# Kernel tuning notes

Hardware: AMD Instinct MI355X
Metric: run time of the kernel (lower is better)

The kernel has to match this reference:

```python
import jax, jax.numpy as jnp
import numpy as np

# DCNv2 config (matches init_kwargs)
STRIDE, PAD, DIL = 1, 1, 1
KH, KW = 3, 3
K = KH * KW


def setup_inputs() -> dict:
    key = jax.random.key(0)
    k1, k2, k3, k4 = jax.random.split(key, 4)
    B, C, H, W = 2, 256, 96, 96
    O = 256
    inp = jax.random.normal(k1, (B, C, H, W), jnp.float32)
    # offset channels interleaved (dy, dx) per kernel tap -> 2*K channels
    offset = jax.random.normal(k2, (B, 2 * K, H, W), jnp.float32)
    # modulation mask in [0,1) (sigmoid is applied outside this module in DCN heads)
    mask = jax.random.uniform(k3, (B, K, H, W), jnp.float32)
    n = C * KH * KW
    stdv = 1.0 / float(np.sqrt(n))
    weight = jax.random.uniform(k4, (O, C, KH, KW), jnp.float32, -stdv, stdv)
    bias = jnp.zeros((O,), jnp.float32)
    return {"input": inp, "offset": offset, "mask": mask, "weight": weight, "bias": bias}


def reference(input, offset, mask, weight, bias):
    B, C, H, W = input.shape
    O = weight.shape[0]
    Ho = (H + 2 * PAD - DIL * (KH - 1) - 1) // STRIDE + 1
    Wo = (W + 2 * PAD - DIL * (KW - 1) - 1) // STRIDE + 1

    # learned per-pixel offsets: channel layout [dy_k0, dx_k0, dy_k1, dx_k1, ...]
    dy = offset[:, 0::2]  # [B,K,Ho,Wo]
    dx = offset[:, 1::2]  # [B,K,Ho,Wo]

    ky = (jnp.arange(K) // KW * DIL).astype(jnp.float32)  # kernel tap row offsets
    kx = (jnp.arange(K) % KW * DIL).astype(jnp.float32)   # kernel tap col offsets
    base_y = (jnp.arange(Ho) * STRIDE - PAD).astype(jnp.float32)
    base_x = (jnp.arange(Wo) * STRIDE - PAD).astype(jnp.float32)

    # sampling positions, [B,K,Ho,Wo]
    y = base_y[None, None, :, None] + ky[None, :, None, None] + dy
    x = base_x[None, None, None, :] + kx[None, :, None, None] + dx

    y0 = jnp.floor(y)
    x0 = jnp.floor(x)
    wy = y - y0  # bilinear fractional weights
    wx = x - x0

    inp_flat = input.reshape(B, C, H * W)

    def gather(yi, xi):
        # zero-padded bilinear corner gather: out-of-bounds -> 0
        ii = yi.astype(jnp.int32)
        jj = xi.astype(jnp.int32)
        valid = ((ii >= 0) & (ii < H) & (jj >= 0) & (jj < W)).astype(input.dtype)
        idx = jnp.clip(ii, 0, H - 1) * W + jnp.clip(jj, 0, W - 1)  # [B,K,Ho,Wo]
        v = jnp.take_along_axis(inp_flat, idx.reshape(B, 1, -1), axis=2)  # [B,C,K*Ho*Wo]
        return v * valid.reshape(B, 1, -1)

    v00 = gather(y0, x0)
    v01 = gather(y0, x0 + 1)
    v10 = gather(y0 + 1, x0)
    v11 = gather(y0 + 1, x0 + 1)

    wyf = wy.reshape(B, 1, -1)
    wxf = wx.reshape(B, 1, -1)
    sampled = (v00 * (1 - wyf) * (1 - wxf) + v01 * (1 - wyf) * wxf
               + v10 * wyf * (1 - wxf) + v11 * wyf * wxf)  # [B,C,K*Ho*Wo]

    mod = sampled * mask.reshape(B, 1, -1)           # modulation per tap/pixel
    mod = mod.reshape(B, C, K, Ho * Wo)
    out = jnp.einsum('bcks,ock->bos', mod, weight.reshape(O, C, K)) + bias[None, :, None]
    return out.reshape(B, O, Ho, Wo)
```

## Files before the change

### kernel.cpp

```cpp
#include <hip/hip_runtime.h>
#include <hip/hip_bf16.h>


#define Hh 96
#define Ww 96
#define Cc 256
#define Oo 256
#define Bb 2
#define Kk 9
#define Ss (Hh * Ww)
#define CKTOT (Cc * Kk)

typedef __bf16 bf16x8 __attribute__((ext_vector_type(8)));
typedef __bf16 bf16x2v __attribute__((ext_vector_type(2)));
typedef float f32x16 __attribute__((ext_vector_type(16)));
typedef float f32x2 __attribute__((ext_vector_type(2)));

__device__ __forceinline__ f32x2 up2(unsigned u) {
  f32x2 r;
  r.x = __uint_as_float(u << 16);
  r.y = __uint_as_float(u & 0xffff0000u);
  return r;
}

__device__ __forceinline__ void barrier_lgkm() {
  asm volatile("" ::: "memory");
  __builtin_amdgcn_s_waitcnt(0xC07F);
  __builtin_amdgcn_s_barrier();
  asm volatile("" ::: "memory");
}

__global__ __launch_bounds__(256) void prep(const float* __restrict__ inp,
                                            const float* __restrict__ wsrc,
                                            __bf16* __restrict__ it,
                                            __bf16* __restrict__ wt) {
  __shared__ float tile[64][65];
  const int bx = blockIdx.x;
  const int tid = threadIdx.x;

  if (bx < 1152) {
    const int hw0 = (bx % 144) * 64;
    const int c0 = ((bx / 144) & 3) * 64;
    const int b = bx / 576;
    const int hw_l = tid & 63, cr = tid >> 6;
    const float* src = inp + ((size_t)(b * Cc + c0) * Ss) + hw0;
#pragma unroll
    for (int r = 0; r < 16; ++r) {
      int c_l = r * 4 + cr;
      tile[c_l][hw_l] = src[(size_t)c_l * Ss + hw_l];
    }
    __syncthreads();
    const int cp = (tid & 31) * 2, hr = tid >> 5;
    __bf16* dst = it + ((size_t)(b * Ss + hw0) * Cc) + c0;
#pragma unroll
    for (int r = 0; r < 8; ++r) {
      int hw_s = r * 8 + hr;
      bf16x2v p;
      p.x = (__bf16)tile[cp][hw_s];
      p.y = (__bf16)tile[cp + 1][hw_s];
      *(bf16x2v*)(dst + (size_t)hw_s * Cc + cp) = p;
    }
  } else {
    int i = (bx - 1152) * 256 + tid;
    int j = i & 7;
    int l = (i >> 3) & 63;
    int osub = (i >> 9) & 7;
    int cc = (i >> 12) & 15;
    int kk = i >> 16;
    int o = osub * 32 + (l & 31);
    int ch = cc * 16 + ((l >> 5) << 3) + j;
    wt[i] = (__bf16)wsrc[(o * Cc + ch) * Kk + kk];
  }
}

__global__ __launch_bounds__(256, 3) void dcn_main(
    const __bf16* __restrict__ it,
    const __bf16* __restrict__ wt,
    const float* __restrict__ offset,
    const float* __restrict__ mask,
    const float* __restrict__ bias,
    float* __restrict__ out)
{
  __shared__ __bf16 colT[2][32 * 256];
  __shared__ int4 pa9[9][32];
  __shared__ float4 pw9[9][32];

  const int tid = threadIdx.x;
  const int tile = (blockIdx.x & 7) * 36 + (blockIdx.x >> 3);
  const int s0 = tile * 32;
  const int b = blockIdx.y;
  const int lane = tid & 63;
  const int wv = tid >> 6;
  const int sB = lane & 31;
  const int hi = lane >> 5;
  const int fs = tid >> 3;
  const int fg = tid & 7;

  const __bf16* itb = it + (size_t)b * Ss * Cc;

  for (int idx = tid; idx < 9 * 32; idx += 256) {
    int kk = idx >> 5;
    int sl = idx & 31;
    int s = s0 + sl;
    int ho = s / Ww;
    int wo = s - ho * Ww;
    float dy = offset[((size_t)(b * 18 + 2 * kk)) * Ss + s];
    float dx = offset[((size_t)(b * 18 + 2 * kk + 1)) * Ss + s];
    float m = mask[((size_t)(b * 9 + kk)) * Ss + s];
    float y = (float)(ho - 1 + kk / 3) + dy;
    float x = (float)(wo - 1 + kk % 3) + dx;
    float fy = floorf(y), fx = floorf(x);
    int y0 = (int)fy, x0 = (int)fx;
    float wy = y - fy, wx = x - fx;
    int y1 = y0 + 1, x1 = x0 + 1;
    float vy0 = (y0 >= 0 && y0 < Hh) ? 1.f : 0.f;
    float vy1 = (y1 >= 0 && y1 < Hh) ? 1.f : 0.f;
    float vx0 = (x0 >= 0 && x0 < Ww) ? 1.f : 0.f;
    float vx1 = (x1 >= 0 && x1 < Ww) ? 1.f : 0.f;
    int y0c = min(max(y0, 0), Hh - 1), y1c = min(max(y1, 0), Hh - 1);
    int x0c = min(max(x0, 0), Ww - 1), x1c = min(max(x1, 0), Ww - 1);
    pa9[kk][sl] = make_int4((y0c * Ww + x0c) * Cc, (y0c * Ww + x1c) * Cc,
                            (y1c * Ww + x0c) * Cc, (y1c * Ww + x1c) * Cc);
    pw9[kk][sl] = make_float4(m * (1.f - wy) * (1.f - wx) * vy0 * vx0,
                              m * (1.f - wy) * wx * vy0 * vx1,
                              m * wy * (1.f - wx) * vy1 * vx0,
                              m * wy * wx * vy1 * vx1);
  }
  __syncthreads();

  f32x16 acc0, acc1;
#pragma unroll
  for (int j = 0; j < 16; ++j) { acc0[j] = 0.f; acc1[j] = 0.f; }

  auto ldW = [&](int kk, int cc, int which) {
    size_t idx = (size_t)((kk * 16 + cc) * 8 + wv * 2 + which);
    return *(const bf16x8*)(wt + (idx << 9) + (lane << 3));
  };
  auto ldB = [&](int buf, int cc) {
    int g = ((2 * cc + hi) ^ (sB & 7)) << 3;
    return *(const bf16x8*)(&colT[buf][sB * 256 + g]);
  };

  for (int kk = 0; kk < Kk; ++kk) {
    const int buf = kk & 1;
    {
      int4 a = pa9[kk][fs];
      float4 wq = pw9[kk][fs];
      __bf16* drow = &colT[buf][fs * 256];
#pragma unroll
      for (int it2 = 0; it2 < 4; ++it2) {
        int g = fg + it2 * 8;
        const __bf16* p = itb + g * 8;
        uint4 c00 = *(const uint4*)(p + a.x);
        uint4 c01 = *(const uint4*)(p + a.y);
        uint4 c10 = *(const uint4*)(p + a.z);
        uint4 c11 = *(const uint4*)(p + a.w);
        unsigned u0[4] = {c00.x, c00.y, c00.z, c00.w};
        unsigned u1[4] = {c01.x, c01.y, c01.z, c01.w};
        unsigned u2[4] = {c10.x, c10.y, c10.z, c10.w};
        unsigned u3[4] = {c11.x, c11.y, c11.z, c11.w};
        bf16x8 rv;
#pragma unroll
        for (int w = 0; w < 4; ++w) {
          f32x2 r = up2(u0[w]) * wq.x + up2(u1[w]) * wq.y +
                    up2(u2[w]) * wq.z + up2(u3[w]) * wq.w;
          rv[2 * w] = (__bf16)r.x;
          rv[2 * w + 1] = (__bf16)r.y;
        }
        *(bf16x8*)(drow + ((g ^ (fs & 7)) << 3)) = rv;
      }
    }
    bf16x8 Wacur = ldW(kk, 0, 0);
    bf16x8 Wbcur = ldW(kk, 0, 1);
    barrier_lgkm();

    bf16x8 Bcur = ldB(buf, 0);
#pragma unroll
    for (int cc = 0; cc < 16; ++cc) {
      bf16x8 Bn, Wan, Wbn;
      if (cc < 15) {
        Bn = ldB(buf, cc + 1);
        Wan = ldW(kk, cc + 1, 0);
        Wbn = ldW(kk, cc + 1, 1);
      }
      acc0 = __builtin_amdgcn_mfma_f32_32x32x16_bf16(Wacur, Bcur, acc0, 0, 0, 0);
      acc1 = __builtin_amdgcn_mfma_f32_32x32x16_bf16(Wbcur, Bcur, acc1, 0, 0, 0);
      if (cc < 15) {
        Bcur = Bn;
        Wacur = Wan;
        Wbcur = Wbn;
      }
    }
  }

  float* ob = out + (size_t)b * Oo * Ss + s0 + sB;
#pragma unroll
  for (int os = 0; os < 2; ++os) {
#pragma unroll
    for (int r = 0; r < 16; ++r) {
      int o = wv * 64 + os * 32 + (r & 3) + 8 * (r >> 2) + 4 * hi;
      float v = (os ? acc1[r] : acc0[r]) + bias[o];
      ob[(size_t)o * Ss] = v;
    }
  }
}

extern "C" void kernel_launch(void* const* d_in, const int* in_sizes, int n_in,
                              void* d_out, int out_size, void* d_ws, size_t ws_size,
                              hipStream_t stream) {
  (void)in_sizes; (void)n_in; (void)out_size; (void)ws_size;
  const float* inp = (const float*)d_in[0];
  const float* offset = (const float*)d_in[1];
  const float* mask = (const float*)d_in[2];
  const float* weight = (const float*)d_in[3];
  const float* bias = (const float*)d_in[4];
  float* out = (float*)d_out;

  __bf16* it = (__bf16*)d_ws;
  __bf16* wt = (__bf16*)((char*)d_ws + (size_t)Bb * Ss * Cc * 2);

  prep<<<3456, 256, 0, stream>>>(inp, weight, it, wt);
  dcn_main<<<dim3(288, Bb), 256, 0, stream>>>(it, wt, offset, mask, bias, out);
}
```

Baseline: 128.1 us.

## Double the spatial tile, use 512 threads, and software-pipeline gathers with MFMA

```diff
diff --git a/kernel.cpp b/kernel.cpp
--- a/kernel.cpp
+++ b/kernel.cpp
@@ -10,6 +10,7 @@
 #define Kk 9
 #define Ss (Hh * Ww)
 #define CKTOT (Cc * Kk)
+#define ROWE 264
 
 typedef __bf16 bf16x8 __attribute__((ext_vector_type(8)));
 typedef __bf16 bf16x2v __attribute__((ext_vector_type(2)));
@@ -64,8 +65,8 @@
     int i = (bx - 1152) * 256 + tid;
     int j = i & 7;
     int l = (i >> 3) & 63;
-    int osub = (i >> 9) & 7;
-    int cc = (i >> 12) & 15;
+    int cc = (i >> 9) & 15;
+    int osub = (i >> 13) & 7;
     int kk = i >> 16;
     int o = osub * 32 + (l & 31);
     int ch = cc * 16 + ((l >> 5) << 3) + j;
@@ -73,7 +74,7 @@
   }
 }
 
-__global__ __launch_bounds__(256, 3) void dcn_main(
+__global__ __launch_bounds__(512, 4) void dcn_main(
     const __bf16* __restrict__ it,
     const __bf16* __restrict__ wt,
     const float* __restrict__ offset,
@@ -81,26 +82,29 @@
     const float* __restrict__ bias,
     float* __restrict__ out)
 {
-  __shared__ __bf16 colT[2][32 * 256];
-  __shared__ int4 pa9[9][32];
-  __shared__ float4 pw9[9][32];
+  __shared__ __bf16 colT[2 * 64 * ROWE];
+  __shared__ ushort4 pp[9][64];
+  __shared__ float4 pwl[9][64];
 
   const int tid = threadIdx.x;
-  const int tile = (blockIdx.x & 7) * 36 + (blockIdx.x >> 3);
-  const int s0 = tile * 32;
+  const int tile = (blockIdx.x & 7) * 18 + (blockIdx.x >> 3);
+  const int s0 = tile * 64;
   const int b = blockIdx.y;
   const int lane = tid & 63;
   const int wv = tid >> 6;
+  const int ow = wv & 3;
+  const int sh = wv >> 2;
   const int sB = lane & 31;
   const int hi = lane >> 5;
+  const int srow = sh * 32 + sB;
   const int fs = tid >> 3;
   const int fg = tid & 7;
 
   const __bf16* itb = it + (size_t)b * Ss * Cc;
 
-  for (int idx = tid; idx < 9 * 32; idx += 256) {
-    int kk = idx >> 5;
-    int sl = idx & 31;
+  for (int idx = tid; idx < 9 * 64; idx += 512) {
+    int kk = idx >> 6;
+    int sl = idx & 63;
     int s = s0 + sl;
     int ho = s / Ww;
     int wo = s - ho * Ww;
@@ -119,9 +123,11 @@
     float vx1 = (x1 >= 0 && x1 < Ww) ? 1.f : 0.f;
     int y0c = min(max(y0, 0), Hh - 1), y1c = min(max(y1, 0), Hh - 1);
     int x0c = min(max(x0, 0), Ww - 1), x1c = min(max(x1, 0), Ww - 1);
-    pa9[kk][sl] = make_int4((y0c * Ww + x0c) * Cc, (y0c * Ww + x1c) * Cc,
-                            (y1c * Ww + x0c) * Cc, (y1c * Ww + x1c) * Cc);
-    pw9[kk][sl] = make_float4(m * (1.f - wy) * (1.f - wx) * vy0 * vx0,
+    pp[kk][sl] = make_ushort4((unsigned short)(y0c * Ww + x0c),
+                              (unsigned short)(y0c * Ww + x1c),
+                              (unsigned short)(y1c * Ww + x0c),
+                              (unsigned short)(y1c * Ww + x1c));
+    pwl[kk][sl] = make_float4(m * (1.f - wy) * (1.f - wx) * vy0 * vx0,
                               m * (1.f - wy) * wx * vy0 * vx1,
                               m * wy * (1.f - wx) * vy1 * vx0,
                               m * wy * wx * vy1 * vx1);
@@ -132,73 +138,128 @@
 #pragma unroll
   for (int j = 0; j < 16; ++j) { acc0[j] = 0.f; acc1[j] = 0.f; }
 
-  auto ldW = [&](int kk, int cc, int which) {
-    size_t idx = (size_t)((kk * 16 + cc) * 8 + wv * 2 + which);
-    return *(const bf16x8*)(wt + (idx << 9) + (lane << 3));
-  };
-  auto ldB = [&](int buf, int cc) {
-    int g = ((2 * cc + hi) ^ (sB & 7)) << 3;
-    return *(const bf16x8*)(&colT[buf][sB * 256 + g]);
-  };
-
-  for (int kk = 0; kk < Kk; ++kk) {
+  unsigned ax0, ax1, ax2, ax3;
+  float4 wq;
+  uint4 D[2][4];
+
+  auto tap_params = [&](int kk) {
+    ushort4 q = pp[kk][fs];
+    wq = pwl[kk][fs];
+    ax0 = (unsigned)q.x << 9;
+    ax1 = (unsigned)q.y << 9;
+    ax2 = (unsigned)q.z << 9;
+    ax3 = (unsigned)q.w << 9;
+  };
+  auto ld_half = [&](int half) {
+    const char* base = (const char*)itb + fg * 16 + half * 256;
+#pragma unroll
+    for (int i2 = 0; i2 < 2; ++i2) {
+      D[i2][0] = *(const uint4*)(base + ax0 + i2 * 128);
+      D[i2][1] = *(const uint4*)(base + ax1 + i2 * 128);
+      D[i2][2] = *(const uint4*)(base + ax2 + i2 * 128);
+      D[i2][3] = *(const uint4*)(base + ax3 + i2 * 128);
+    }
+  };
+  auto bil_half = [&](int tb, int half) {
+    __bf16* drow = colT + tb * (64 * ROWE) + fs * ROWE + fg * 8 + half * 128;
+#pragma unroll
+    for (int i2 = 0; i2 < 2; ++i2) {
+      unsigned u0[4] = {D[i2][0].x, D[i2][0].y, D[i2][0].z, D[i2][0].w};
+      unsigned u1[4] = {D[i2][1].x, D[i2][1].y, D[i2][1].z, D[i2][1].w};
+      unsigned u2[4] = {D[i2][2].x, D[i2][2].y, D[i2][2].z, D[i2][2].w};
+      unsigned u3[4] = {D[i2][3].x, D[i2][3].y, D[i2][3].z, D[i2][3].w};
+      bf16x8 rv;
+#pragma unroll
+      for (int w = 0; w < 4; ++w) {
+        f32x2 r = up2(u0[w]) * wq.x + up2(u1[w]) * wq.y +
+                  up2(u2[w]) * wq.z + up2(u3[w]) * wq.w;
+        rv[2 * w] = (__bf16)r.x;
+        rv[2 * w + 1] = (__bf16)r.y;
+      }
+      *(bf16x8*)(drow + i2 * 64) = rv;
+    }
+  };
+
+  auto wbaseA = [&](int kk) {
+    return wt + (((size_t)kk * 8 + ow * 2) << 13) + lane * 8;
+  };
+  auto wbaseB = [&](int kk) {
+    return wt + (((size_t)kk * 8 + ow * 2 + 1) << 13) + lane * 8;
+  };
+
+  tap_params(0);
+  ld_half(0);
+  bil_half(0, 0);
+  ld_half(1);
+  bil_half(0, 1);
+  bf16x8 WAc = *(const bf16x8*)wbaseA(0);
+  bf16x8 WBc = *(const bf16x8*)wbaseB(0);
+
+  for (int kk = 0; kk < 8; ++kk) {
+    barrier_lgkm();
     const int buf = kk & 1;
-    {
-      int4 a = pa9[kk][fs];
-      float4 wq = pw9[kk][fs];
-      __bf16* drow = &colT[buf][fs * 256];
-#pragma unroll
-      for (int it2 = 0; it2 < 4; ++it2) {
-        int g = fg + it2 * 8;
-        const __bf16* p = itb + g * 8;
-        uint4 c00 = *(const uint4*)(p + a.x);
-        uint4 c01 = *(const uint4*)(p + a.y);
-        uint4 c10 = *(const uint4*)(p + a.z);
-        uint4 c11 = *(const uint4*)(p + a.w);
-        unsigned u0[4] = {c00.x, c00.y, c00.z, c00.w};
-        unsigned u1[4] = {c01.x, c01.y, c01.z, c01.w};
-        unsigned u2[4] = {c10.x, c10.y, c10.z, c10.w};
-        unsigned u3[4] = {c11.x, c11.y, c11.z, c11.w};
-        bf16x8 rv;
-#pragma unroll
-        for (int w = 0; w < 4; ++w) {
-          f32x2 r = up2(u0[w]) * wq.x + up2(u1[w]) * wq.y +
-                    up2(u2[w]) * wq.z + up2(u3[w]) * wq.w;
-          rv[2 * w] = (__bf16)r.x;
-          rv[2 * w + 1] = (__bf16)r.y;
-        }
-        *(bf16x8*)(drow + ((g ^ (fs & 7)) << 3)) = rv;
-      }
-    }
-    bf16x8 Wacur = ldW(kk, 0, 0);
-    bf16x8 Wbcur = ldW(kk, 0, 1);
-    barrier_lgkm();
-
-    bf16x8 Bcur = ldB(buf, 0);
+    tap_params(kk + 1);
+    ld_half(0);
+
+    const __bf16* rp = colT + buf * (64 * ROWE) + srow * ROWE + hi * 8;
+    const __bf16* pA = wbaseA(kk);
+    const __bf16* pB = wbaseB(kk);
+    bf16x8 Bc = *(const bf16x8*)rp;
 #pragma unroll
     for (int cc = 0; cc < 16; ++cc) {
-      bf16x8 Bn, Wan, Wbn;
-      if (cc < 15) {
-        Bn = ldB(buf, cc + 1);
-        Wan = ldW(kk, cc + 1, 0);
-        Wbn = ldW(kk, cc + 1, 1);
-      }
-      acc0 = __builtin_amdgcn_mfma_f32_32x32x16_bf16(Wacur, Bcur, acc0, 0, 0, 0);
-      acc1 = __builtin_amdgcn_mfma_f32_32x32x16_bf16(Wbcur, Bcur, acc1, 0, 0, 0);
-      if (cc < 15) {
-        Bcur = Bn;
-        Wacur = Wan;
-        Wbcur = Wbn;
-      }
-    }
-  }
-
-  float* ob = out + (size_t)b * Oo * Ss + s0 + sB;
+      bf16x8 Bn, WAn, WBn;
+      if (cc < 15) {
+        Bn = *(const bf16x8*)(rp + (cc + 1) * 16);
+        WAn = *(const bf16x8*)(pA + (cc + 1) * 512);
+        WBn = *(const bf16x8*)(pB + (cc + 1) * 512);
+      }
+      acc0 = __builtin_amdgcn_mfma_f32_32x32x16_bf16(WAc, Bc, acc0, 0, 0, 0);
+      acc1 = __builtin_amdgcn_mfma_f32_32x32x16_bf16(WBc, Bc, acc1, 0, 0, 0);
+      if (cc == 7) {
+        bil_half(buf ^ 1, 0);
+        ld_half(1);
+      }
+      if (cc < 15) {
+        Bc = Bn;
+        WAc = WAn;
+        WBc = WBn;
+      }
+    }
+    bil_half(buf ^ 1, 1);
+    WAc = *(const bf16x8*)wbaseA(kk + 1);
+    WBc = *(const bf16x8*)wbaseB(kk + 1);
+  }
+
+  barrier_lgkm();
+  {
+    const __bf16* rp = colT + 0 * (64 * ROWE) + srow * ROWE + hi * 8;
+    const __bf16* pA = wbaseA(8);
+    const __bf16* pB = wbaseB(8);
+    bf16x8 Bc = *(const bf16x8*)rp;
+#pragma unroll
+    for (int cc = 0; cc < 16; ++cc) {
+      bf16x8 Bn, WAn, WBn;
+      if (cc < 15) {
+        Bn = *(const bf16x8*)(rp + (cc + 1) * 16);
+        WAn = *(const bf16x8*)(pA + (cc + 1) * 512);
+        WBn = *(const bf16x8*)(pB + (cc + 1) * 512);
+      }
+      acc0 = __builtin_amdgcn_mfma_f32_32x32x16_bf16(WAc, Bc, acc0, 0, 0, 0);
+      acc1 = __builtin_amdgcn_mfma_f32_32x32x16_bf16(WBc, Bc, acc1, 0, 0, 0);
+      if (cc < 15) {
+        Bc = Bn;
+        WAc = WAn;
+        WBc = WBn;
+      }
+    }
+  }
+
+  float* ob = out + (size_t)b * Oo * Ss + s0 + srow;
 #pragma unroll
   for (int os = 0; os < 2; ++os) {
 #pragma unroll
     for (int r = 0; r < 16; ++r) {
-      int o = wv * 64 + os * 32 + (r & 3) + 8 * (r >> 2) + 4 * hi;
+      int o = ow * 64 + os * 32 + (r & 3) + 8 * (r >> 2) + 4 * hi;
       float v = (os ? acc1[r] : acc0[r]) + bias[o];
       ob[(size_t)o * Ss] = v;
     }
@@ -220,5 +281,5 @@
   __bf16* wt = (__bf16*)((char*)d_ws + (size_t)Bb * Ss * Cc * 2);
 
   prep<<<3456, 256, 0, stream>>>(inp, weight, it, wt);
-  dcn_main<<<dim3(288, Bb), 256, 0, stream>>>(it, wt, offset, mask, bias, out);
-}
+  dcn_main<<<dim3(144, Bb), 512, 0, stream>>>(it, wt, offset, mask, bias, out);
+}
```

Measured after the change: 141.9 us. +10.8%, slower.

## Single-buffer LDS tile, deepen weight prefetch, reorder weight layout, raise occupancy

Applied to the files above, without the earlier changes.

```diff
diff --git a/kernel.cpp b/kernel.cpp
--- a/kernel.cpp
+++ b/kernel.cpp
@@ -64,8 +64,8 @@
     int i = (bx - 1152) * 256 + tid;
     int j = i & 7;
     int l = (i >> 3) & 63;
-    int osub = (i >> 9) & 7;
-    int cc = (i >> 12) & 15;
+    int cc = (i >> 9) & 15;
+    int osub = (i >> 13) & 7;
     int kk = i >> 16;
     int o = osub * 32 + (l & 31);
     int ch = cc * 16 + ((l >> 5) << 3) + j;
@@ -73,7 +73,7 @@
   }
 }
 
-__global__ __launch_bounds__(256, 3) void dcn_main(
+__global__ __launch_bounds__(256, 4) void dcn_main(
     const __bf16* __restrict__ it,
     const __bf16* __restrict__ wt,
     const float* __restrict__ offset,
@@ -81,7 +81,7 @@
     const float* __restrict__ bias,
     float* __restrict__ out)
 {
-  __shared__ __bf16 colT[2][32 * 256];
+  __shared__ __bf16 colB[32 * 32 * 8];
   __shared__ int4 pa9[9][32];
   __shared__ float4 pw9[9][32];
 
@@ -93,10 +93,10 @@
   const int wv = tid >> 6;
   const int sB = lane & 31;
   const int hi = lane >> 5;
-  const int fs = tid >> 3;
-  const int fg = tid & 7;
-
-  const __bf16* itb = it + (size_t)b * Ss * Cc;
+  const int fs = tid & 31;
+  const int gb = ((tid >> 5) & 1) + ((tid >> 6) << 1);
+
+  const char* itb = (const char*)(it + (size_t)b * Ss * Cc);
 
   for (int idx = tid; idx < 9 * 32; idx += 256) {
     int kk = idx >> 5;
@@ -119,8 +119,8 @@
     float vx1 = (x1 >= 0 && x1 < Ww) ? 1.f : 0.f;
     int y0c = min(max(y0, 0), Hh - 1), y1c = min(max(y1, 0), Hh - 1);
     int x0c = min(max(x0, 0), Ww - 1), x1c = min(max(x1, 0), Ww - 1);
-    pa9[kk][sl] = make_int4((y0c * Ww + x0c) * Cc, (y0c * Ww + x1c) * Cc,
-                            (y1c * Ww + x0c) * Cc, (y1c * Ww + x1c) * Cc);
+    pa9[kk][sl] = make_int4((y0c * Ww + x0c) << 9, (y0c * Ww + x1c) << 9,
+                            (y1c * Ww + x0c) << 9, (y1c * Ww + x1c) << 9);
     pw9[kk][sl] = make_float4(m * (1.f - wy) * (1.f - wx) * vy0 * vx0,
                               m * (1.f - wy) * wx * vy0 * vx1,
                               m * wy * (1.f - wx) * vy1 * vx0,
@@ -132,64 +132,70 @@
 #pragma unroll
   for (int j = 0; j < 16; ++j) { acc0[j] = 0.f; acc1[j] = 0.f; }
 
-  auto ldW = [&](int kk, int cc, int which) {
-    size_t idx = (size_t)((kk * 16 + cc) * 8 + wv * 2 + which);
-    return *(const bf16x8*)(wt + (idx << 9) + (lane << 3));
-  };
-  auto ldB = [&](int buf, int cc) {
-    int g = ((2 * cc + hi) ^ (sB & 7)) << 3;
-    return *(const bf16x8*)(&colT[buf][sB * 256 + g]);
-  };
-
   for (int kk = 0; kk < Kk; ++kk) {
-    const int buf = kk & 1;
+    if (kk) barrier_lgkm();
+
+    const __bf16* pA = wt + (((size_t)(kk * 8 + wv * 2) * 16) << 9) + lane * 8;
+    const __bf16* pB2 = pA + (16 << 9);
+    bf16x8 WA0 = *(const bf16x8*)(pA);
+    bf16x8 WB0 = *(const bf16x8*)(pB2);
+    bf16x8 WA1 = *(const bf16x8*)(pA + 512);
+    bf16x8 WB1 = *(const bf16x8*)(pB2 + 512);
+    bf16x8 WA2 = *(const bf16x8*)(pA + 1024);
+    bf16x8 WB2 = *(const bf16x8*)(pB2 + 1024);
+
     {
       int4 a = pa9[kk][fs];
       float4 wq = pw9[kk][fs];
-      __bf16* drow = &colT[buf][fs * 256];
-#pragma unroll
-      for (int it2 = 0; it2 < 4; ++it2) {
-        int g = fg + it2 * 8;
-        const __bf16* p = itb + g * 8;
-        uint4 c00 = *(const uint4*)(p + a.x);
-        uint4 c01 = *(const uint4*)(p + a.y);
-        uint4 c10 = *(const uint4*)(p + a.z);
-        uint4 c11 = *(const uint4*)(p + a.w);
-        unsigned u0[4] = {c00.x, c00.y, c00.z, c00.w};
-        unsigned u1[4] = {c01.x, c01.y, c01.z, c01.w};
-        unsigned u2[4] = {c10.x, c10.y, c10.z, c10.w};
-        unsigned u3[4] = {c11.x, c11.y, c11.z, c11.w};
-        bf16x8 rv;
-#pragma unroll
-        for (int w = 0; w < 4; ++w) {
-          f32x2 r = up2(u0[w]) * wq.x + up2(u1[w]) * wq.y +
-                    up2(u2[w]) * wq.z + up2(u3[w]) * wq.w;
-          rv[2 * w] = (__bf16)r.x;
-          rv[2 * w + 1] = (__bf16)r.y;
+#pragma unroll
+      for (int half = 0; half < 2; ++half) {
+        uint4 D[2][4];
+#pragma unroll
+        for (int q = 0; q < 2; ++q) {
+          int g = gb + (half * 2 + q) * 8;
+          const char* p = itb + g * 16;
+          D[q][0] = *(const uint4*)(p + a.x);
+          D[q][1] = *(const uint4*)(p + a.y);
+          D[q][2] = *(const uint4*)(p + a.z);
+          D[q][3] = *(const uint4*)(p + a.w);
         }
-        *(bf16x8*)(drow + ((g ^ (fs & 7)) << 3)) = rv;
+#pragma unroll
+        for (int q = 0; q < 2; ++q) {
+          int g = gb + (half * 2 + q) * 8;
+          unsigned u0[4] = {D[q][0].x, D[q][0].y, D[q][0].z, D[q][0].w};
+          unsigned u1[4] = {D[q][1].x, D[q][1].y, D[q][1].z, D[q][1].w};
+          unsigned u2[4] = {D[q][2].x, D[q][2].y, D[q][2].z, D[q][2].w};
+          unsigned u3[4] = {D[q][3].x, D[q][3].y, D[q][3].z, D[q][3].w};
+          bf16x8 rv;
+#pragma unroll
+          for (int w = 0; w < 4; ++w) {
+            f32x2 r = up2(u0[w]) * wq.x + up2(u1[w]) * wq.y +
+                      up2(u2[w]) * wq.z + up2(u3[w]) * wq.w;
+            rv[2 * w] = (__bf16)r.x;
+            rv[2 * w + 1] = (__bf16)r.y;
+          }
+          *(bf16x8*)&colB[(g * 32 + fs) * 8] = rv;
+        }
       }
     }
-    bf16x8 Wacur = ldW(kk, 0, 0);
-    bf16x8 Wbcur = ldW(kk, 0, 1);
     barrier_lgkm();
 
-    bf16x8 Bcur = ldB(buf, 0);
-#pragma unroll
-    for (int cc = 0; cc < 16; ++cc) {
-      bf16x8 Bn, Wan, Wbn;
-      if (cc < 15) {
-        Bn = ldB(buf, cc + 1);
-        Wan = ldW(kk, cc + 1, 0);
-        Wbn = ldW(kk, cc + 1, 1);
+    const __bf16* bp = &colB[(hi * 32 + sB) * 8];
+    bf16x8 Bc = *(const bf16x8*)bp;
+#pragma unroll
+    for (int c = 0; c < 16; ++c) {
+      bf16x8 Bn, WAn, WBn;
+      if (c < 15) Bn = *(const bf16x8*)(bp + (c + 1) * 512);
+      if (c < 13) {
+        WAn = *(const bf16x8*)(pA + (c + 3) * 512);
+        WBn = *(const bf16x8*)(pB2 + (c + 3) * 512);
       }
-      acc0 = __builtin_amdgcn_mfma_f32_32x32x16_bf16(Wacur, Bcur, acc0, 0, 0, 0);
-      acc1 = __builtin_amdgcn_mfma_f32_32x32x16_bf16(Wbcur, Bcur, acc1, 0, 0, 0);
-      if (cc < 15) {
-        Bcur = Bn;
-        Wacur = Wan;
-        Wbcur = Wbn;
-      }
+      acc0 = __builtin_amdgcn_mfma_f32_32x32x16_bf16(WA0, Bc, acc0, 0, 0, 0);
+      acc1 = __builtin_amdgcn_mfma_f32_32x32x16_bf16(WB0, Bc, acc1, 0, 0, 0);
+      WA0 = WA1; WB0 = WB1;
+      WA1 = WA2; WB1 = WB2;
+      if (c < 13) { WA2 = WAn; WB2 = WBn; }
+      if (c < 15) Bc = Bn;
     }
   }
 
```

Measured after the change: 157.7 us. +23.1%, slower.
